# Performance work log

Measured on AMD Instinct MI355X. Metric: run time of the kernel, lower is better.

The kernel has to match this reference:

```python
import jax, jax.numpy as jnp
import numpy as np

N_NODES = 100000
N_EDGES = 600000
D = 128


def setup_inputs() -> dict:
    key = jax.random.key(0)
    ks = jax.random.split(key, 12)
    inp = {
        'feat': jax.random.normal(ks[0], (N_NODES, D), dtype=jnp.float32),
        'W_tran': jax.random.normal(ks[1], (D, D), dtype=jnp.float32) * (1.0 / np.sqrt(D)),
        'att_w1': jax.random.normal(ks[2], (4 * D, D), dtype=jnp.float32) * (1.0 / np.sqrt(D)),
        'att_b1': jax.random.normal(ks[3], (4 * D,), dtype=jnp.float32) * 0.01,
        'att_w2': jax.random.normal(ks[4], (1, 4 * D), dtype=jnp.float32) * (1.0 / np.sqrt(4 * D)),
        'trans_w': jax.random.uniform(ks[5], (N_EDGES,), dtype=jnp.float32),
        'geo_src': jax.random.randint(ks[6], (N_EDGES,), 0, N_NODES, dtype=jnp.int32),
        'geo_dst': jax.random.randint(ks[7], (N_EDGES,), 0, N_NODES, dtype=jnp.int32),
        'cat_src': jax.random.randint(ks[8], (N_EDGES,), 0, N_NODES, dtype=jnp.int32),
        'cat_dst': jax.random.randint(ks[9], (N_EDGES,), 0, N_NODES, dtype=jnp.int32),
        'trans_src': jax.random.randint(ks[10], (N_EDGES,), 0, N_NODES, dtype=jnp.int32),
        'trans_dst': jax.random.randint(ks[11], (N_EDGES,), 0, N_NODES, dtype=jnp.int32),
    }
    return inp


def _mean_agg(f, src, dst, n):
    # copy_u('f','m') then mean('m', .) : gather src feats, segment-mean by dst
    msum = jax.ops.segment_sum(f[src], dst, num_segments=n)
    cnt = jax.ops.segment_sum(jnp.ones((src.shape[0],), f.dtype), dst, num_segments=n)
    return msum / jnp.maximum(cnt, 1.0)[:, None]


def reference(feat, W_tran, att_w1, att_b1, att_w2, trans_w,
              geo_src, geo_dst, cat_src, cat_dst, trans_src, trans_dst):
    n = feat.shape[0]
    # feat_tran: Linear(D, D, bias=False) -> x @ W^T
    f = feat @ W_tran.T
    geo = _mean_agg(f, geo_src, geo_dst, n)            # [N, D]
    cat = _mean_agg(f, cat_src, cat_dst, n)            # [N, D]
    # u_mul_e('f','w') then sum: weighted gather + segment-sum by dst
    trans = jax.ops.segment_sum(f[trans_src] * trans_w[:, None], trans_dst, num_segments=n)
    z = jnp.stack([geo, trans, cat], axis=1)           # [N, 3, D]
    # SemanticAttention: Linear -> tanh -> Linear(no bias), mean over nodes, softmax over relations
    h = jnp.tanh(jnp.einsum('nrd,hd->nrh', z, att_w1) + att_b1)   # [N, 3, 4D]
    w = jnp.einsum('nrh,oh->nro', h, att_w2).mean(0)              # [3, 1]
    beta = jax.nn.softmax(w, axis=0)                              # [3, 1]
    fused = (beta[None, :, :] * z).sum(1)                         # [N, D]
    return jax.nn.leaky_relu(fused, negative_slope=0.2)
```

## Files before the change

kernel.cpp:

```cpp
#include <hip/hip_runtime.h>
#include <math.h>

#define DD 128
#define NNODES 100000
#define NEDGES 600000
#define NREL 3
#define MTOT (NREL*NNODES)
#define NTILES (NNODES/16)
#define RT_PER_BLK 8
#define NBLK_REL ((NTILES + RT_PER_BLK - 1)/RT_PER_BLK)
#define ATT_WAVES 8

#define BSHIFT 10
#define NBUCK ((NNODES + 1023) >> BSHIFT)
#define GBUCK (NREL*NBUCK)
#define CAP 8192
#define P1_THREADS 512
#define P1_EPT 8
#define P1_EPB (P1_THREADS*P1_EPT)
#define P1_BLOCKS ((NREL*NEDGES + P1_EPB - 1)/P1_EPB)

typedef __attribute__((ext_vector_type(8))) short short8;
typedef __attribute__((ext_vector_type(4))) float f32x4;

__device__ inline float bf2f(unsigned short u){ return __uint_as_float(((unsigned int)u)<<16); }
__device__ inline float bflo(unsigned int u){ return __uint_as_float(u<<16); }
__device__ inline float bfhi(unsigned int u){ return __uint_as_float(u & 0xffff0000u); }
__device__ inline unsigned short f2bf(float f){
    unsigned int i = __float_as_uint(f);
    unsigned int r = (i + 0x7fffu + ((i>>16)&1u)) >> 16;
    return (unsigned short)r;
}
__device__ inline unsigned int pack2(float lo, float hi){
    return (unsigned int)f2bf(lo) | ((unsigned int)f2bf(hi) << 16);
}
__device__ inline short8 cvt8(const float* __restrict__ p){
    f32x4 a = *(const f32x4*)p;
    f32x4 b = *(const f32x4*)(p+4);
    short8 t;
    t[0]=(short)f2bf(a[0]); t[1]=(short)f2bf(a[1]); t[2]=(short)f2bf(a[2]); t[3]=(short)f2bf(a[3]);
    t[4]=(short)f2bf(b[0]); t[5]=(short)f2bf(b[1]); t[6]=(short)f2bf(b[2]); t[7]=(short)f2bf(b[3]);
    return t;
}
__device__ inline void acc8(float* a, float w, uint4 v){
    a[0] += w*bflo(v.x); a[1] += w*bfhi(v.x);
    a[2] += w*bflo(v.y); a[3] += w*bfhi(v.y);
    a[4] += w*bflo(v.z); a[5] += w*bfhi(v.z);
    a[6] += w*bflo(v.w); a[7] += w*bfhi(v.w);
}

__global__ __launch_bounds__(256) void k_cvt2(
    const float* __restrict__ ina, unsigned short* __restrict__ outa, int na4,
    const float* __restrict__ inb, unsigned short* __restrict__ outb, int nb4)
{
    int gid = blockIdx.x*256 + threadIdx.x;
    const float* in; unsigned short* out; int idx;
    if (gid < na4){ in = ina; out = outa; idx = gid; }
    else { idx = gid - na4; if (idx >= nb4) return; in = inb; out = outb; }
    f32x4 v = ((const f32x4*)in)[idx];
    ushort4 o;
    o.x=f2bf(v[0]); o.y=f2bf(v[1]); o.z=f2bf(v[2]); o.w=f2bf(v[3]);
    ((ushort4*)out)[idx] = o;
}

__global__ __launch_bounds__(256) void k_transform(
    const float* __restrict__ feat, const unsigned short* __restrict__ Wbf,
    unsigned short* __restrict__ f_out)
{
    int wid = blockIdx.x*4 + (threadIdx.x>>6);
    if (wid >= NNODES/16) return;
    int lane = threadIdx.x & 63;
    int m = lane & 15, quad = lane >> 4;
    int n0 = wid*16;

    short8 a[4];
    const float* arow = feat + (size_t)(n0+m)*DD;
    #pragma unroll
    for (int ks=0; ks<4; ++ks) a[ks] = cvt8(arow + ks*32 + quad*8);

    #pragma unroll
    for (int ct=0; ct<8; ++ct){
        f32x4 acc = {0.f,0.f,0.f,0.f};
        const short8* brow = (const short8*)(Wbf + (size_t)(ct*16+m)*DD);
        #pragma unroll
        for (int ks=0; ks<4; ++ks){
            acc = __builtin_amdgcn_mfma_f32_16x16x32_bf16(a[ks], brow[ks*4+quad], acc, 0,0,0);
        }
        int col = ct*16 + m;
        #pragma unroll
        for (int i=0;i<4;++i)
            f_out[(size_t)(n0+quad*4+i)*DD + col] = f2bf(acc[i]);
    }
}

__global__ __launch_bounds__(P1_THREADS) void k_part(
    const int* __restrict__ s0, const int* __restrict__ d0,
    const int* __restrict__ s1, const int* __restrict__ d1,
    const int* __restrict__ s2, const int* __restrict__ d2,
    const float* __restrict__ tw,
    int* __restrict__ bcur,
    int2* __restrict__ slab, float* __restrict__ wslab)
{
    __shared__ int hist[GBUCK];
    for (int i=threadIdx.x; i<GBUCK; i+=P1_THREADS) hist[i]=0;
    __syncthreads();

    int e0 = blockIdx.x * P1_EPB;
    int ss[P1_EPT], dd_[P1_EPT], gb[P1_EPT]; float wv[P1_EPT];
    #pragma unroll
    for (int j=0;j<P1_EPT;++j){
        int e = e0 + j*P1_THREADS + threadIdx.x;
        gb[j] = -1;
        if (e < NREL*NEDGES){
            int rel = e / NEDGES; int i = e - rel*NEDGES;
            const int* s = (rel==0)?s0:(rel==1)?s1:s2;
            const int* d = (rel==0)?d0:(rel==1)?d1:d2;
            ss[j]=s[i]; dd_[j]=d[i];
            wv[j] = (rel==2)? tw[i] : 0.f;
            gb[j] = rel*NBUCK + (dd_[j]>>BSHIFT);
            atomicAdd(&hist[gb[j]], 1);
        }
    }
    __syncthreads();
    for (int i=threadIdx.x; i<GBUCK; i+=P1_THREADS){
        int c = hist[i];
        hist[i] = (c>0) ? atomicAdd(&bcur[i], c) : 0;
    }
    __syncthreads();
    #pragma unroll
    for (int j=0;j<P1_EPT;++j){
        if (gb[j] >= 0){
            int off = atomicAdd(&hist[gb[j]], 1);
            int2 pr; pr.x = ss[j]; pr.y = dd_[j];
            slab[(size_t)gb[j]*CAP + off] = pr;
            if (gb[j] >= 2*NBUCK) wslab[(size_t)(gb[j]-2*NBUCK)*CAP + off] = wv[j];
        }
    }
}

__global__ __launch_bounds__(512) void k_csr(
    const int2* __restrict__ slab, const float* __restrict__ wslab,
    const int* __restrict__ bcur,
    int* __restrict__ offs, int* __restrict__ cnt,
    int* __restrict__ es, float* __restrict__ ewt)
{
    __shared__ int lcnt[1024];
    __shared__ int lsc[1024];
    __shared__ int psum[512];
    int gb = blockIdx.x;
    int rel = gb / NBUCK, b = gb - rel*NBUCK;
    int n0 = b << BSHIFT;
    int nn = min(1024, NNODES - n0);
    int ecount = bcur[gb];
    const int2* ep = slab + (size_t)gb*CAP;
    int t = threadIdx.x;

    psum[t] = (t < gb) ? bcur[t] : 0;
    __syncthreads();
    for (int off=256; off; off>>=1){
        if (t < off) psum[t] += psum[t+off];
        __syncthreads();
    }
    int base = psum[0];
    __syncthreads();

    lcnt[2*t] = 0; lcnt[2*t+1] = 0;
    __syncthreads();
    for (int i=t; i<ecount; i+=512)
        atomicAdd(&lcnt[ep[i].y - n0], 1);
    __syncthreads();
    int v0 = lcnt[2*t], v1 = lcnt[2*t+1];
    psum[t] = v0 + v1; __syncthreads();
    for (int off=1; off<512; off<<=1){
        int x = (t>=off)? psum[t-off] : 0;
        __syncthreads(); psum[t]+=x; __syncthreads();
    }
    int ex = (t>0)? psum[t-1] : 0;
    lsc[2*t] = ex; lsc[2*t+1] = ex + v0;
    __syncthreads();
    int relN = rel*NNODES;
    for (int i=t; i<nn; i+=512){
        offs[relN + n0 + i] = base + lsc[i];
        cnt [relN + n0 + i] = lcnt[i];
    }
    __syncthreads();
    for (int i=t; i<ecount; i+=512){
        int2 pr = ep[i];
        int pos = base + atomicAdd(&lsc[pr.y - n0], 1);
        es[pos] = pr.x;
        if (rel==2) ewt[pos - 2*NEDGES] = wslab[(size_t)b*CAP + i];
    }
}

__global__ __launch_bounds__(256) void k_agg_u(
    const unsigned short* __restrict__ f,
    const int* __restrict__ es,
    const int* __restrict__ offs, const int* __restrict__ cnt,
    unsigned short* __restrict__ z)
{
    int gid = blockIdx.x*256 + threadIdx.x;
    int g = gid >> 4;
    if (g >= 2*NNODES) return;
    int c = gid & 15;
    int start = offs[g];
    int deg   = cnt[g];

    float a[8] = {0,0,0,0,0,0,0,0};
    int i = 0;
    for (; i+3 < deg; i += 4){
        int s0 = es[start+i],   s1 = es[start+i+1];
        int s2 = es[start+i+2], s3 = es[start+i+3];
        uint4 v0 = *(const uint4*)(f + (size_t)s0*DD + c*8);
        uint4 v1 = *(const uint4*)(f + (size_t)s1*DD + c*8);
        uint4 v2 = *(const uint4*)(f + (size_t)s2*DD + c*8);
        uint4 v3 = *(const uint4*)(f + (size_t)s3*DD + c*8);
        acc8(a, 1.f, v0); acc8(a, 1.f, v1); acc8(a, 1.f, v2); acc8(a, 1.f, v3);
    }
    if (i+1 < deg){
        int s0 = es[start+i], s1 = es[start+i+1];
        uint4 v0 = *(const uint4*)(f + (size_t)s0*DD + c*8);
        uint4 v1 = *(const uint4*)(f + (size_t)s1*DD + c*8);
        acc8(a, 1.f, v0); acc8(a, 1.f, v1);
        i += 2;
    }
    if (i < deg){
        int s = es[start+i];
        uint4 v = *(const uint4*)(f + (size_t)s*DD + c*8);
        acc8(a, 1.f, v);
    }
    float sc = 1.f/fmaxf((float)deg, 1.f);
    uint4 o;
    o.x = pack2(a[0]*sc, a[1]*sc);
    o.y = pack2(a[2]*sc, a[3]*sc);
    o.z = pack2(a[4]*sc, a[5]*sc);
    o.w = pack2(a[6]*sc, a[7]*sc);
    *(uint4*)(z + (size_t)g*DD + c*8) = o;
}

__global__ __launch_bounds__(256) void k_agg_w(
    const unsigned short* __restrict__ f,
    const int* __restrict__ es, const float* __restrict__ ewt,
    const int* __restrict__ offs, const int* __restrict__ cnt,
    unsigned short* __restrict__ z)
{
    int gid = blockIdx.x*256 + threadIdx.x;
    int g = (gid >> 4) + 2*NNODES;
    if (g >= MTOT) return;
    int c = gid & 15;
    int start = offs[g];
    int deg   = cnt[g];

    float a[8] = {0,0,0,0,0,0,0,0};
    int i = 0;
    for (; i+3 < deg; i += 4){
        int s0 = es[start+i],   s1 = es[start+i+1];
        int s2 = es[start+i+2], s3 = es[start+i+3];
        float w0 = ewt[start+i   - 2*NEDGES];
        float w1 = ewt[start+i+1 - 2*NEDGES];
        float w2 = ewt[start+i+2 - 2*NEDGES];
        float w3 = ewt[start+i+3 - 2*NEDGES];
        uint4 v0 = *(const uint4*)(f + (size_t)s0*DD + c*8);
        uint4 v1 = *(const uint4*)(f + (size_t)s1*DD + c*8);
        uint4 v2 = *(const uint4*)(f + (size_t)s2*DD + c*8);
        uint4 v3 = *(const uint4*)(f + (size_t)s3*DD + c*8);
        acc8(a, w0, v0); acc8(a, w1, v1); acc8(a, w2, v2); acc8(a, w3, v3);
    }
    if (i+1 < deg){
        int s0 = es[start+i], s1 = es[start+i+1];
        float w0 = ewt[start+i   - 2*NEDGES];
        float w1 = ewt[start+i+1 - 2*NEDGES];
        uint4 v0 = *(const uint4*)(f + (size_t)s0*DD + c*8);
        uint4 v1 = *(const uint4*)(f + (size_t)s1*DD + c*8);
        acc8(a, w0, v0); acc8(a, w1, v1);
        i += 2;
    }
    if (i < deg){
        int s = es[start+i];
        float w = ewt[start+i - 2*NEDGES];
        uint4 v = *(const uint4*)(f + (size_t)s*DD + c*8);
        acc8(a, w, v);
    }
    uint4 o;
    o.x = pack2(a[0], a[1]);
    o.y = pack2(a[2], a[3]);
    o.z = pack2(a[4], a[5]);
    o.w = pack2(a[6], a[7]);
    *(uint4*)(z + (size_t)g*DD + c*8) = o;
}

__global__ __launch_bounds__(512, 4) void k_att(
    const unsigned short* __restrict__ z,
    const unsigned short* __restrict__ w1,
    const float* __restrict__ bias1,
    const float* __restrict__ wv2,
    float* __restrict__ w_part)
{
    __shared__ uint4 sm[RT_PER_BLK*256];
    __shared__ float sred[ATT_WAVES];
    const float C2 = 2.8853900817779268f;

    int rel = blockIdx.x / NBLK_REL;
    int nb  = blockIdx.x % NBLK_REL;
    int trt0 = nb * RT_PER_BLK;
    int rt_count = min(RT_PER_BLK, NTILES - trt0);
    int row0 = trt0 * 16;
    const unsigned short* zrel = z + (size_t)rel*NNODES*DD;

    int lane = threadIdx.x & 63;
    int wv   = threadIdx.x >> 6;
    int m = lane & 15, quad = lane >> 4;

    short8 bq[16];
    float ww[4], bbc[4];
    #pragma unroll
    for (int ct=0; ct<4; ++ct){
        int col = (wv*4 + ct)*16 + m;
        const short8* brow = (const short8*)(w1 + (size_t)col*DD);
        #pragma unroll
        for (int ks=0; ks<4; ++ks) bq[ct*4+ks] = brow[ks*4 + quad];
        ww[ct]  = wv2[col];
        bbc[ct] = bias1[col] * C2;
    }

    int valid_rows = rt_count * 16;
    #pragma unroll
    for (int i=0; i<4; ++i){
        int u = i*512 + threadIdx.x;
        int row = u >> 4, kc = u & 15;
        if (row < valid_rows){
            uint4 v = *(const uint4*)(zrel + (size_t)(row0+row)*DD + kc*8);
            int rt = row >> 4, mm = row & 15;
            sm[rt*256 + kc*16 + (mm ^ kc)] = v;
        }
    }
    __syncthreads();

    const short8* smx = (const short8*)sm;
    float s_r[4] = {0.f,0.f,0.f,0.f};
    for (int rt=0; rt<rt_count; ++rt){
        int base = rt*256;
        short8 a0 = smx[base + (0  + quad)*16 + (m ^ (0  + quad))];
        short8 a1 = smx[base + (4  + quad)*16 + (m ^ (4  + quad))];
        short8 a2 = smx[base + (8  + quad)*16 + (m ^ (8  + quad))];
        short8 a3 = smx[base + (12 + quad)*16 + (m ^ (12 + quad))];
        #pragma unroll
        for (int ct=0; ct<4; ++ct){
            f32x4 acc = {0.f,0.f,0.f,0.f};
            acc = __builtin_amdgcn_mfma_f32_16x16x32_bf16(a0, bq[ct*4+0], acc, 0,0,0);
            acc = __builtin_amdgcn_mfma_f32_16x16x32_bf16(a1, bq[ct*4+1], acc, 0,0,0);
            acc = __builtin_amdgcn_mfma_f32_16x16x32_bf16(a2, bq[ct*4+2], acc, 0,0,0);
            acc = __builtin_amdgcn_mfma_f32_16x16x32_bf16(a3, bq[ct*4+3], acc, 0,0,0);
            #pragma unroll
            for (int i=0;i<4;++i){
                float e = __builtin_amdgcn_exp2f(__builtin_fmaf(acc[i], C2, bbc[ct]));
                s_r[ct] += __builtin_amdgcn_rcpf(e + 1.f);
            }
        }
    }
    float s_all = 0.f;
    #pragma unroll
    for (int ct=0; ct<4; ++ct)
        s_all += ww[ct]*(float)(4*rt_count) - 2.f*ww[ct]*s_r[ct];
    #pragma unroll
    for (int off=32; off; off>>=1) s_all += __shfl_xor(s_all, off);
    if (lane == 0) sred[wv] = s_all;
    __syncthreads();
    if (threadIdx.x == 0){
        float tt = 0.f;
        #pragma unroll
        for (int i=0;i<ATT_WAVES;++i) tt += sred[i];
        atomicAdd(&w_part[rel], tt);
    }
}

__global__ __launch_bounds__(256) void k_final(
    const unsigned short* __restrict__ z0, const unsigned short* __restrict__ z1,
    const unsigned short* __restrict__ z2,
    const float* __restrict__ w_part, float* __restrict__ out)
{
    int gid = blockIdx.x*256 + threadIdx.x;
    if (gid >= NNODES*DD/4) return;
    const float invN = 1.f / (float)NNODES;
    float w0 = w_part[0]*invN, w1 = w_part[1]*invN, w2 = w_part[2]*invN;
    float mx = fmaxf(w0, fmaxf(w1, w2));
    const float LOG2E = 1.4426950408889634f;
    float e0 = __builtin_amdgcn_exp2f((w0-mx)*LOG2E);
    float e1 = __builtin_amdgcn_exp2f((w1-mx)*LOG2E);
    float e2 = __builtin_amdgcn_exp2f((w2-mx)*LOG2E);
    float inv = 1.f/(e0+e1+e2);
    float b0 = e0*inv, b1 = e1*inv, b2 = e2*inv;
    ushort4 g = ((const ushort4*)z0)[gid];
    ushort4 t = ((const ushort4*)z1)[gid];
    ushort4 c = ((const ushort4*)z2)[gid];
    f32x4 o;
    float gv[4] = {bf2f(g.x),bf2f(g.y),bf2f(g.z),bf2f(g.w)};
    float tv[4] = {bf2f(t.x),bf2f(t.y),bf2f(t.z),bf2f(t.w)};
    float cv[4] = {bf2f(c.x),bf2f(c.y),bf2f(c.z),bf2f(c.w)};
    #pragma unroll
    for (int i=0;i<4;++i){
        float x = b0*gv[i] + b1*tv[i] + b2*cv[i];
        o[i] = (x > 0.f) ? x : 0.2f*x;
    }
    ((f32x4*)out)[gid] = o;
}

extern "C" void kernel_launch(void* const* d_in, const int* in_sizes, int n_in,
                              void* d_out, int out_size, void* d_ws, size_t ws_size,
                              hipStream_t stream)
{
    const float* feat = (const float*)d_in[0];
    const float* W    = (const float*)d_in[1];
    const float* aw1  = (const float*)d_in[2];
    const float* ab1  = (const float*)d_in[3];
    const float* aw2  = (const float*)d_in[4];
    const float* tw   = (const float*)d_in[5];
    const int* geo_src   = (const int*)d_in[6];
    const int* geo_dst   = (const int*)d_in[7];
    const int* cat_src   = (const int*)d_in[8];
    const int* cat_dst   = (const int*)d_in[9];
    const int* trans_src = (const int*)d_in[10];
    const int* trans_dst = (const int*)d_in[11];

    char* ws = (char*)d_ws;
    float* w_part = (float*)ws;
    int*   bcur   = (int*)(w_part + 64);
    int*   offs   = bcur + 320;
    int*   cnt    = offs + MTOT;
    unsigned short* w1_bf = (unsigned short*)(cnt + MTOT);
    unsigned short* w_bf  = w1_bf + 512*DD;
    int*   es     = (int*)(w_bf + DD*DD);
    float* ewt    = (float*)(es + NREL*NEDGES);
    unsigned short* z = (unsigned short*)(ewt + NEDGES);
    int2*  slab   = (int2*)z;
    float* wslab  = (float*)(slab + (size_t)GBUCK*CAP);
    unsigned short* f_bf = (unsigned short*)d_out;

    (void)hipMemsetAsync(w_part, 0, (64 + 320)*sizeof(int), stream);

    int na4 = 512*DD/4, nb4 = DD*DD/4;
    k_cvt2<<<(na4 + nb4 + 255)/256, 256, 0, stream>>>(aw1, w1_bf, na4, W, w_bf, nb4);
    k_transform<<<(NNODES/16 + 3)/4, 256, 0, stream>>>(feat, w_bf, f_bf);

    k_part<<<P1_BLOCKS, P1_THREADS, 0, stream>>>(geo_src, geo_dst, cat_src, cat_dst,
                                                 trans_src, trans_dst, tw,
                                                 bcur, slab, wslab);
    k_csr<<<GBUCK, 512, 0, stream>>>(slab, wslab, bcur, offs, cnt, es, ewt);

    k_agg_u<<<(2*NNODES*16 + 255)/256, 256, 0, stream>>>(f_bf, es, offs, cnt, z);
    k_agg_w<<<(NNODES*16 + 255)/256, 256, 0, stream>>>(f_bf, es, ewt, offs, cnt, z);

    k_att<<<NREL*NBLK_REL, 512, 0, stream>>>(z, w1_bf, ab1, aw2, w_part);

    unsigned short* z_geo   = z;
    unsigned short* z_cat   = z + (size_t)NNODES*DD;
    unsigned short* z_trans = z + (size_t)2*NNODES*DD;
    int dg = (NNODES*DD/4 + 255)/256;
    k_final<<<dg, 256, 0, stream>>>(z_geo, z_cat, z_trans, w_part, (float*)d_out);
}
```

Measured before the change: 357.5 us.

## Fuse front-end kernels into one launch, merge aggregations, halve CSR buckets

Combines the edge partition, the feature transform (now converting W to bf16 inline) and the attention-weight conversion into a single heterogeneous launch, so they overlap and launch overhead drops. The two aggregation kernels become one launch. Bucket size halves to 512 nodes with a smaller slab capacity, which doubles the CSR block count for more parallelism. This risks slab overflow if a bucket exceeds 4096 edges, and it adds redundant W conversion in each transform wave.

```diff
diff --git a/kernel.cpp b/kernel.cpp
--- a/kernel.cpp
+++ b/kernel.cpp
@@ -11,14 +11,21 @@
 #define NBLK_REL ((NTILES + RT_PER_BLK - 1)/RT_PER_BLK)
 #define ATT_WAVES 8
 
-#define BSHIFT 10
-#define NBUCK ((NNODES + 1023) >> BSHIFT)
+#define BSHIFT 9
+#define NBUCK ((NNODES + 511) >> BSHIFT)
 #define GBUCK (NREL*NBUCK)
-#define CAP 8192
+#define CAP 4096
 #define P1_THREADS 512
 #define P1_EPT 8
 #define P1_EPB (P1_THREADS*P1_EPT)
 #define P1_BLOCKS ((NREL*NEDGES + P1_EPB - 1)/P1_EPB)
+
+#define TR_BLOCKS ((NTILES + 7)/8)
+#define CVT_BLOCKS ((512*DD/4 + 511)/512)
+#define FRONT_BLOCKS (P1_BLOCKS + TR_BLOCKS + CVT_BLOCKS)
+
+#define AGGU_BLOCKS ((2*NNODES*16)/256)
+#define AGGW_BLOCKS ((NNODES*16)/256)
 
 typedef __attribute__((ext_vector_type(8))) short short8;
 typedef __attribute__((ext_vector_type(4))) float f32x4;
@@ -49,91 +56,87 @@
     a[6] += w*bflo(v.w); a[7] += w*bfhi(v.w);
 }
 
-__global__ __launch_bounds__(256) void k_cvt2(
-    const float* __restrict__ ina, unsigned short* __restrict__ outa, int na4,
-    const float* __restrict__ inb, unsigned short* __restrict__ outb, int nb4)
-{
-    int gid = blockIdx.x*256 + threadIdx.x;
-    const float* in; unsigned short* out; int idx;
-    if (gid < na4){ in = ina; out = outa; idx = gid; }
-    else { idx = gid - na4; if (idx >= nb4) return; in = inb; out = outb; }
-    f32x4 v = ((const f32x4*)in)[idx];
-    ushort4 o;
-    o.x=f2bf(v[0]); o.y=f2bf(v[1]); o.z=f2bf(v[2]); o.w=f2bf(v[3]);
-    ((ushort4*)out)[idx] = o;
-}
-
-__global__ __launch_bounds__(256) void k_transform(
-    const float* __restrict__ feat, const unsigned short* __restrict__ Wbf,
-    unsigned short* __restrict__ f_out)
-{
-    int wid = blockIdx.x*4 + (threadIdx.x>>6);
-    if (wid >= NNODES/16) return;
-    int lane = threadIdx.x & 63;
-    int m = lane & 15, quad = lane >> 4;
-    int n0 = wid*16;
-
-    short8 a[4];
-    const float* arow = feat + (size_t)(n0+m)*DD;
-    #pragma unroll
-    for (int ks=0; ks<4; ++ks) a[ks] = cvt8(arow + ks*32 + quad*8);
-
-    #pragma unroll
-    for (int ct=0; ct<8; ++ct){
-        f32x4 acc = {0.f,0.f,0.f,0.f};
-        const short8* brow = (const short8*)(Wbf + (size_t)(ct*16+m)*DD);
-        #pragma unroll
-        for (int ks=0; ks<4; ++ks){
-            acc = __builtin_amdgcn_mfma_f32_16x16x32_bf16(a[ks], brow[ks*4+quad], acc, 0,0,0);
-        }
-        int col = ct*16 + m;
-        #pragma unroll
-        for (int i=0;i<4;++i)
-            f_out[(size_t)(n0+quad*4+i)*DD + col] = f2bf(acc[i]);
-    }
-}
-
-__global__ __launch_bounds__(P1_THREADS) void k_part(
+__global__ __launch_bounds__(512) void k_front(
+    const float* __restrict__ feat, const float* __restrict__ W,
+    const float* __restrict__ aw1,
     const int* __restrict__ s0, const int* __restrict__ d0,
     const int* __restrict__ s1, const int* __restrict__ d1,
     const int* __restrict__ s2, const int* __restrict__ d2,
     const float* __restrict__ tw,
-    int* __restrict__ bcur,
-    int2* __restrict__ slab, float* __restrict__ wslab)
+    int* __restrict__ bcur, int2* __restrict__ slab, float* __restrict__ wslab,
+    unsigned short* __restrict__ w1_bf, unsigned short* __restrict__ f_out)
 {
     __shared__ int hist[GBUCK];
-    for (int i=threadIdx.x; i<GBUCK; i+=P1_THREADS) hist[i]=0;
-    __syncthreads();
-
-    int e0 = blockIdx.x * P1_EPB;
-    int ss[P1_EPT], dd_[P1_EPT], gb[P1_EPT]; float wv[P1_EPT];
-    #pragma unroll
-    for (int j=0;j<P1_EPT;++j){
-        int e = e0 + j*P1_THREADS + threadIdx.x;
-        gb[j] = -1;
-        if (e < NREL*NEDGES){
-            int rel = e / NEDGES; int i = e - rel*NEDGES;
-            const int* s = (rel==0)?s0:(rel==1)?s1:s2;
-            const int* d = (rel==0)?d0:(rel==1)?d1:d2;
-            ss[j]=s[i]; dd_[j]=d[i];
-            wv[j] = (rel==2)? tw[i] : 0.f;
-            gb[j] = rel*NBUCK + (dd_[j]>>BSHIFT);
-            atomicAdd(&hist[gb[j]], 1);
-        }
-    }
-    __syncthreads();
-    for (int i=threadIdx.x; i<GBUCK; i+=P1_THREADS){
-        int c = hist[i];
-        hist[i] = (c>0) ? atomicAdd(&bcur[i], c) : 0;
-    }
-    __syncthreads();
-    #pragma unroll
-    for (int j=0;j<P1_EPT;++j){
-        if (gb[j] >= 0){
-            int off = atomicAdd(&hist[gb[j]], 1);
-            int2 pr; pr.x = ss[j]; pr.y = dd_[j];
-            slab[(size_t)gb[j]*CAP + off] = pr;
-            if (gb[j] >= 2*NBUCK) wslab[(size_t)(gb[j]-2*NBUCK)*CAP + off] = wv[j];
+    int bid = blockIdx.x;
+
+    if (bid < P1_BLOCKS){
+        for (int i=threadIdx.x; i<GBUCK; i+=512) hist[i]=0;
+        __syncthreads();
+
+        int e0 = bid * P1_EPB;
+        int ss[P1_EPT], dd_[P1_EPT], gb[P1_EPT]; float wv[P1_EPT];
+        #pragma unroll
+        for (int j=0;j<P1_EPT;++j){
+            int e = e0 + j*512 + threadIdx.x;
+            gb[j] = -1;
+            if (e < NREL*NEDGES){
+                int rel = e / NEDGES; int i = e - rel*NEDGES;
+                const int* s = (rel==0)?s0:(rel==1)?s1:s2;
+                const int* d = (rel==0)?d0:(rel==1)?d1:d2;
+                ss[j]=s[i]; dd_[j]=d[i];
+                wv[j] = (rel==2)? tw[i] : 0.f;
+                gb[j] = rel*NBUCK + (dd_[j]>>BSHIFT);
+                atomicAdd(&hist[gb[j]], 1);
+            }
+        }
+        __syncthreads();
+        for (int i=threadIdx.x; i<GBUCK; i+=512){
+            int c = hist[i];
+            hist[i] = (c>0) ? atomicAdd(&bcur[i], c) : 0;
+        }
+        __syncthreads();
+        #pragma unroll
+        for (int j=0;j<P1_EPT;++j){
+            if (gb[j] >= 0){
+                int off = atomicAdd(&hist[gb[j]], 1);
+                int2 pr; pr.x = ss[j]; pr.y = dd_[j];
+                slab[(size_t)gb[j]*CAP + off] = pr;
+                if (gb[j] >= 2*NBUCK) wslab[(size_t)(gb[j]-2*NBUCK)*CAP + off] = wv[j];
+            }
+        }
+    } else if (bid < P1_BLOCKS + TR_BLOCKS){
+        int wid = (bid - P1_BLOCKS)*8 + (threadIdx.x>>6);
+        if (wid >= NTILES) return;
+        int lane = threadIdx.x & 63;
+        int m = lane & 15, quad = lane >> 4;
+        int n0 = wid*16;
+
+        short8 a[4];
+        const float* arow = feat + (size_t)(n0+m)*DD;
+        #pragma unroll
+        for (int ks=0; ks<4; ++ks) a[ks] = cvt8(arow + ks*32 + quad*8);
+
+        #pragma unroll
+        for (int ct=0; ct<8; ++ct){
+            f32x4 acc = {0.f,0.f,0.f,0.f};
+            const float* brow = W + (size_t)(ct*16+m)*DD;
+            #pragma unroll
+            for (int ks=0; ks<4; ++ks){
+                short8 b = cvt8(brow + ks*32 + quad*8);
+                acc = __builtin_amdgcn_mfma_f32_16x16x32_bf16(a[ks], b, acc, 0,0,0);
+            }
+            int col = ct*16 + m;
+            #pragma unroll
+            for (int i=0;i<4;++i)
+                f_out[(size_t)(n0+quad*4+i)*DD + col] = f2bf(acc[i]);
+        }
+    } else {
+        int gid = (bid - P1_BLOCKS - TR_BLOCKS)*512 + threadIdx.x;
+        if (gid < 512*DD/4){
+            f32x4 v = ((const f32x4*)aw1)[gid];
+            ushort4 o;
+            o.x=f2bf(v[0]); o.y=f2bf(v[1]); o.z=f2bf(v[2]); o.w=f2bf(v[3]);
+            ((ushort4*)w1_bf)[gid] = o;
         }
     }
 }
@@ -144,19 +147,20 @@
     int* __restrict__ offs, int* __restrict__ cnt,
     int* __restrict__ es, float* __restrict__ ewt)
 {
-    __shared__ int lcnt[1024];
-    __shared__ int lsc[1024];
+    __shared__ int lcnt[512];
+    __shared__ int lsc[512];
     __shared__ int psum[512];
     int gb = blockIdx.x;
     int rel = gb / NBUCK, b = gb - rel*NBUCK;
     int n0 = b << BSHIFT;
-    int nn = min(1024, NNODES - n0);
+    int nn = min(512, NNODES - n0);
     int ecount = bcur[gb];
     const int2* ep = slab + (size_t)gb*CAP;
     int t = threadIdx.x;
 
-    psum[t] = (t < gb) ? bcur[t] : 0;
-    __syncthreads();
+    int acc = (t < gb) ? bcur[t] : 0;
+    if (t + 512 < gb) acc += bcur[t + 512];
+    psum[t] = acc; __syncthreads();
     for (int off=256; off; off>>=1){
         if (t < off) psum[t] += psum[t+off];
         __syncthreads();
@@ -164,26 +168,23 @@
     int base = psum[0];
     __syncthreads();
 
-    lcnt[2*t] = 0; lcnt[2*t+1] = 0;
-    __syncthreads();
+    lcnt[t] = 0; __syncthreads();
     for (int i=t; i<ecount; i+=512)
         atomicAdd(&lcnt[ep[i].y - n0], 1);
     __syncthreads();
-    int v0 = lcnt[2*t], v1 = lcnt[2*t+1];
-    psum[t] = v0 + v1; __syncthreads();
+    int v = lcnt[t];
+    psum[t] = v; __syncthreads();
     for (int off=1; off<512; off<<=1){
         int x = (t>=off)? psum[t-off] : 0;
-        __syncthreads(); psum[t]+=x; __syncthreads();
+        __syncthreads(); psum[t] += x; __syncthreads();
     }
     int ex = (t>0)? psum[t-1] : 0;
-    lsc[2*t] = ex; lsc[2*t+1] = ex + v0;
+    lsc[t] = ex;
     __syncthreads();
-    int relN = rel*NNODES;
-    for (int i=t; i<nn; i+=512){
-        offs[relN + n0 + i] = base + lsc[i];
-        cnt [relN + n0 + i] = lcnt[i];
-    }
-    __syncthreads();
+    if (t < nn){
+        offs[rel*NNODES + n0 + t] = base + ex;
+        cnt [rel*NNODES + n0 + t] = v;
+    }
     for (int i=t; i<ecount; i+=512){
         int2 pr = ep[i];
         int pos = base + atomicAdd(&lsc[pr.y - n0], 1);
@@ -192,100 +193,92 @@
     }
 }
 
-__global__ __launch_bounds__(256) void k_agg_u(
-    const unsigned short* __restrict__ f,
-    const int* __restrict__ es,
-    const int* __restrict__ offs, const int* __restrict__ cnt,
-    unsigned short* __restrict__ z)
-{
-    int gid = blockIdx.x*256 + threadIdx.x;
-    int g = gid >> 4;
-    if (g >= 2*NNODES) return;
-    int c = gid & 15;
-    int start = offs[g];
-    int deg   = cnt[g];
-
-    float a[8] = {0,0,0,0,0,0,0,0};
-    int i = 0;
-    for (; i+3 < deg; i += 4){
-        int s0 = es[start+i],   s1 = es[start+i+1];
-        int s2 = es[start+i+2], s3 = es[start+i+3];
-        uint4 v0 = *(const uint4*)(f + (size_t)s0*DD + c*8);
-        uint4 v1 = *(const uint4*)(f + (size_t)s1*DD + c*8);
-        uint4 v2 = *(const uint4*)(f + (size_t)s2*DD + c*8);
-        uint4 v3 = *(const uint4*)(f + (size_t)s3*DD + c*8);
-        acc8(a, 1.f, v0); acc8(a, 1.f, v1); acc8(a, 1.f, v2); acc8(a, 1.f, v3);
-    }
-    if (i+1 < deg){
-        int s0 = es[start+i], s1 = es[start+i+1];
-        uint4 v0 = *(const uint4*)(f + (size_t)s0*DD + c*8);
-        uint4 v1 = *(const uint4*)(f + (size_t)s1*DD + c*8);
-        acc8(a, 1.f, v0); acc8(a, 1.f, v1);
-        i += 2;
-    }
-    if (i < deg){
-        int s = es[start+i];
-        uint4 v = *(const uint4*)(f + (size_t)s*DD + c*8);
-        acc8(a, 1.f, v);
-    }
-    float sc = 1.f/fmaxf((float)deg, 1.f);
-    uint4 o;
-    o.x = pack2(a[0]*sc, a[1]*sc);
-    o.y = pack2(a[2]*sc, a[3]*sc);
-    o.z = pack2(a[4]*sc, a[5]*sc);
-    o.w = pack2(a[6]*sc, a[7]*sc);
-    *(uint4*)(z + (size_t)g*DD + c*8) = o;
-}
-
-__global__ __launch_bounds__(256) void k_agg_w(
+__global__ __launch_bounds__(256) void k_agg(
     const unsigned short* __restrict__ f,
     const int* __restrict__ es, const float* __restrict__ ewt,
     const int* __restrict__ offs, const int* __restrict__ cnt,
     unsigned short* __restrict__ z)
 {
-    int gid = blockIdx.x*256 + threadIdx.x;
-    int g = (gid >> 4) + 2*NNODES;
-    if (g >= MTOT) return;
-    int c = gid & 15;
-    int start = offs[g];
-    int deg   = cnt[g];
-
-    float a[8] = {0,0,0,0,0,0,0,0};
-    int i = 0;
-    for (; i+3 < deg; i += 4){
-        int s0 = es[start+i],   s1 = es[start+i+1];
-        int s2 = es[start+i+2], s3 = es[start+i+3];
-        float w0 = ewt[start+i   - 2*NEDGES];
-        float w1 = ewt[start+i+1 - 2*NEDGES];
-        float w2 = ewt[start+i+2 - 2*NEDGES];
-        float w3 = ewt[start+i+3 - 2*NEDGES];
-        uint4 v0 = *(const uint4*)(f + (size_t)s0*DD + c*8);
-        uint4 v1 = *(const uint4*)(f + (size_t)s1*DD + c*8);
-        uint4 v2 = *(const uint4*)(f + (size_t)s2*DD + c*8);
-        uint4 v3 = *(const uint4*)(f + (size_t)s3*DD + c*8);
-        acc8(a, w0, v0); acc8(a, w1, v1); acc8(a, w2, v2); acc8(a, w3, v3);
-    }
-    if (i+1 < deg){
-        int s0 = es[start+i], s1 = es[start+i+1];
-        float w0 = ewt[start+i   - 2*NEDGES];
-        float w1 = ewt[start+i+1 - 2*NEDGES];
-        uint4 v0 = *(const uint4*)(f + (size_t)s0*DD + c*8);
-        uint4 v1 = *(const uint4*)(f + (size_t)s1*DD + c*8);
-        acc8(a, w0, v0); acc8(a, w1, v1);
-        i += 2;
-    }
-    if (i < deg){
-        int s = es[start+i];
-        float w = ewt[start+i - 2*NEDGES];
-        uint4 v = *(const uint4*)(f + (size_t)s*DD + c*8);
-        acc8(a, w, v);
-    }
-    uint4 o;
-    o.x = pack2(a[0], a[1]);
-    o.y = pack2(a[2], a[3]);
-    o.z = pack2(a[4], a[5]);
-    o.w = pack2(a[6], a[7]);
-    *(uint4*)(z + (size_t)g*DD + c*8) = o;
+    int bid = blockIdx.x;
+    if (bid < AGGU_BLOCKS){
+        int gid = bid*256 + threadIdx.x;
+        int g = gid >> 4;
+        int c = gid & 15;
+        int start = offs[g];
+        int deg   = cnt[g];
+        float a[8] = {0,0,0,0,0,0,0,0};
+        int i = 0;
+        for (; i+3 < deg; i += 4){
+            int s0 = es[start+i],   s1 = es[start+i+1];
+            int s2 = es[start+i+2], s3 = es[start+i+3];
+            uint4 v0 = *(const uint4*)(f + (size_t)s0*DD + c*8);
+            uint4 v1 = *(const uint4*)(f + (size_t)s1*DD + c*8);
+            uint4 v2 = *(const uint4*)(f + (size_t)s2*DD + c*8);
+            uint4 v3 = *(const uint4*)(f + (size_t)s3*DD + c*8);
+            acc8(a, 1.f, v0); acc8(a, 1.f, v1); acc8(a, 1.f, v2); acc8(a, 1.f, v3);
+        }
+        if (i+1 < deg){
+            int s0 = es[start+i], s1 = es[start+i+1];
+            uint4 v0 = *(const uint4*)(f + (size_t)s0*DD + c*8);
+            uint4 v1 = *(const uint4*)(f + (size_t)s1*DD + c*8);
+            acc8(a, 1.f, v0); acc8(a, 1.f, v1);
+            i += 2;
+        }
+        if (i < deg){
+            int s = es[start+i];
+            uint4 v = *(const uint4*)(f + (size_t)s*DD + c*8);
+            acc8(a, 1.f, v);
+        }
+        float sc = 1.f/fmaxf((float)deg, 1.f);
+        uint4 o;
+        o.x = pack2(a[0]*sc, a[1]*sc);
+        o.y = pack2(a[2]*sc, a[3]*sc);
+        o.z = pack2(a[4]*sc, a[5]*sc);
+        o.w = pack2(a[6]*sc, a[7]*sc);
+        *(uint4*)(z + (size_t)g*DD + c*8) = o;
+    } else {
+        int gid = (bid - AGGU_BLOCKS)*256 + threadIdx.x;
+        int g = (gid >> 4) + 2*NNODES;
+        int c = gid & 15;
+        int start = offs[g];
+        int deg   = cnt[g];
+        float a[8] = {0,0,0,0,0,0,0,0};
+        int i = 0;
+        for (; i+3 < deg; i += 4){
+            int s0 = es[start+i],   s1 = es[start+i+1];
+            int s2 = es[start+i+2], s3 = es[start+i+3];
+            float w0 = ewt[start+i   - 2*NEDGES];
+            float w1 = ewt[start+i+1 - 2*NEDGES];
+            float w2 = ewt[start+i+2 - 2*NEDGES];
+            float w3 = ewt[start+i+3 - 2*NEDGES];
+            uint4 v0 = *(const uint4*)(f + (size_t)s0*DD + c*8);
+            uint4 v1 = *(const uint4*)(f + (size_t)s1*DD + c*8);
+            uint4 v2 = *(const uint4*)(f + (size_t)s2*DD + c*8);
+            uint4 v3 = *(const uint4*)(f + (size_t)s3*DD + c*8);
+            acc8(a, w0, v0); acc8(a, w1, v1); acc8(a, w2, v2); acc8(a, w3, v3);
+        }
+        if (i+1 < deg){
+            int s0 = es[start+i], s1 = es[start+i+1];
+            float w0 = ewt[start+i   - 2*NEDGES];
+            float w1 = ewt[start+i+1 - 2*NEDGES];
+            uint4 v0 = *(const uint4*)(f + (size_t)s0*DD + c*8);
+            uint4 v1 = *(const uint4*)(f + (size_t)s1*DD + c*8);
+            acc8(a, w0, v0); acc8(a, w1, v1);
+            i += 2;
+        }
+        if (i < deg){
+            int s = es[start+i];
+            float w = ewt[start+i - 2*NEDGES];
+            uint4 v = *(const uint4*)(f + (size_t)s*DD + c*8);
+            acc8(a, w, v);
+        }
+        uint4 o;
+        o.x = pack2(a[0], a[1]);
+        o.y = pack2(a[2], a[3]);
+        o.z = pack2(a[4], a[5]);
+        o.w = pack2(a[6], a[7]);
+        *(uint4*)(z + (size_t)g*DD + c*8) = o;
+    }
 }
 
 __global__ __launch_bounds__(512, 4) void k_att(
@@ -424,30 +417,26 @@
     char* ws = (char*)d_ws;
     float* w_part = (float*)ws;
     int*   bcur   = (int*)(w_part + 64);
-    int*   offs   = bcur + 320;
+    int*   offs   = bcur + 640;
     int*   cnt    = offs + MTOT;
     unsigned short* w1_bf = (unsigned short*)(cnt + MTOT);
-    unsigned short* w_bf  = w1_bf + 512*DD;
-    int*   es     = (int*)(w_bf + DD*DD);
+    int*   es     = (int*)(w1_bf + 512*DD);
     float* ewt    = (float*)(es + NREL*NEDGES);
     unsigned short* z = (unsigned short*)(ewt + NEDGES);
     int2*  slab   = (int2*)z;
     float* wslab  = (float*)(slab + (size_t)GBUCK*CAP);
     unsigned short* f_bf = (unsigned short*)d_out;
 
-    (void)hipMemsetAsync(w_part, 0, (64 + 320)*sizeof(int), stream);
-
-    int na4 = 512*DD/4, nb4 = DD*DD/4;
-    k_cvt2<<<(na4 + nb4 + 255)/256, 256, 0, stream>>>(aw1, w1_bf, na4, W, w_bf, nb4);
-    k_transform<<<(NNODES/16 + 3)/4, 256, 0, stream>>>(feat, w_bf, f_bf);
-
-    k_part<<<P1_BLOCKS, P1_THREADS, 0, stream>>>(geo_src, geo_dst, cat_src, cat_dst,
-                                                 trans_src, trans_dst, tw,
-                                                 bcur, slab, wslab);
+    (void)hipMemsetAsync(w_part, 0, (64 + 640)*sizeof(int), stream);
+
+    k_front<<<FRONT_BLOCKS, 512, 0, stream>>>(feat, W, aw1,
+                                              geo_src, geo_dst, cat_src, cat_dst,
+                                              trans_src, trans_dst, tw,
+                                              bcur, slab, wslab, w1_bf, f_bf);
+
     k_csr<<<GBUCK, 512, 0, stream>>>(slab, wslab, bcur, offs, cnt, es, ewt);
 
-    k_agg_u<<<(2*NNODES*16 + 255)/256, 256, 0, stream>>>(f_bf, es, offs, cnt, z);
-    k_agg_w<<<(NNODES*16 + 255)/256, 256, 0, stream>>>(f_bf, es, ewt, offs, cnt, z);
+    k_agg<<<AGGU_BLOCKS + AGGW_BLOCKS, 256, 0, stream>>>(f_bf, es, ewt, offs, cnt, z);
 
     k_att<<<NREL*NBLK_REL, 512, 0, stream>>>(z, w1_bf, ab1, aw2, w_part);
 
```

Measured after the change: 358.7 us. No clear change (+0.3%).
